# Performance work log

Measured on AMD Instinct MI355X. Metric: run time of the kernel, lower is better.

Reference implementation:

```python
import jax, jax.numpy as jnp
import numpy as np

EMBED, HIDDEN, VOCAB = 512, 512, 30000
B, S, K, NT = 16, 128, 49, 5


def _lin(x, W, b):
    # torch nn.Linear: y = x @ W.T + b, W stored as (out, in)
    return x @ W.T + b


def setup_inputs() -> dict:
    key = jax.random.key(0)
    ks = jax.random.split(key, 32)
    g = lambda i, shape, scale=0.05: (jax.random.normal(ks[i], shape, dtype=jnp.float32) * scale)
    inp = {
        "epoch": 30,
        "h_t": jax.random.normal(ks[0], (B, S, HIDDEN), dtype=jnp.float32),
        "V": jax.random.normal(ks[1], (B, K, HIDDEN), dtype=jnp.float32),
        "T": jax.random.normal(ks[2], (B, NT, EMBED), dtype=jnp.float32),
        "W_ZV": g(3, (49, HIDDEN)), "b_ZV": jnp.zeros((49,), jnp.float32),
        "W_Zh": g(4, (49, HIDDEN)), "b_Zh": jnp.zeros((49,), jnp.float32),
        "W_az": g(5, (1, 49)), "b_az": jnp.zeros((1,), jnp.float32),
        "W_QT": g(6, (5, EMBED)), "b_QT": jnp.zeros((5,), jnp.float32),
        "W_Qh": g(7, (5, HIDDEN)), "b_Qh": jnp.zeros((5,), jnp.float32),
        "W_bq": g(8, (1, 5)), "b_bq": jnp.zeros((1,), jnp.float32),
        "W_sq": g(9, (EMBED, EMBED)), "b_sq": jnp.zeros((EMBED,), jnp.float32),
        "W_sh": g(10, (EMBED, HIDDEN)), "b_sh": jnp.zeros((EMBED,), jnp.float32),
        "W_Ss": g(11, (5, EMBED)), "b_Ss": jnp.zeros((5,), jnp.float32),
        "W_Sr": g(12, (5, EMBED)), "b_Sr": jnp.zeros((5,), jnp.float32),
        "W_sz": g(13, (EMBED, HIDDEN)), "b_sz": jnp.zeros((EMBED,), jnp.float32),
        "W_mlp": g(14, (VOCAB, EMBED)), "b_mlp": jnp.zeros((VOCAB,), jnp.float32),
    }
    return inp


def reference(epoch, h_t, V, T,
              W_ZV, b_ZV, W_Zh, b_Zh, W_az, b_az,
              W_QT, b_QT, W_Qh, b_Qh, W_bq, b_bq,
              W_sq, b_sq, W_sh, b_sh, W_Ss, b_Ss,
              W_Sr, b_Sr, W_sz, b_sz, W_mlp, b_mlp):
    # --- visual attention (dropout = identity, eval mode) ---
    # content_V: [B, S, K, 49]
    content_V = _lin(V, W_ZV, b_ZV)[:, None, :, :] + _lin(h_t, W_Zh, b_Zh)[:, :, None, :]
    visual_t = (jnp.tanh(content_V) @ W_az.T + b_az)[..., 0]          # [B, S, K]
    alpha_t = jax.nn.softmax(visual_t, axis=-1)
    z_t = jnp.einsum('bsk,bkh->bsh', alpha_t, V)                      # [B, S, H]
    r_t = jnp.tanh(_lin(z_t, W_sz, b_sz))                             # [B, S, E]
    # --- topic attention ---
    content_T = _lin(T, W_QT, b_QT)[:, None, :, :] + _lin(h_t, W_Qh, b_Qh)[:, :, None, :]  # [B,S,5,5]
    topic_t = (jnp.tanh(content_T) @ W_bq.T + b_bq)[..., 0]           # [B, S, 5]
    beta_t = jax.nn.softmax(topic_t, axis=-1)
    q_t = jnp.einsum('bst,bte->bse', beta_t, T)                       # [B, S, E]
    s_t = jnp.tanh(_lin(q_t, W_sq, b_sq) + _lin(h_t, W_sh, b_sh))     # [B, S, E]
    # --- sentinel scores: the torch loop reduces to (batch 0, diagonal pos) only ---
    qh0 = _lin(h_t[0], W_Qh, b_Qh)                                    # [S, 5]
    score_s = jnp.tanh(_lin(s_t[0], W_Ss, b_Ss) + qh0) @ W_bq.T + b_bq  # [S, 1]
    score_r = jnp.tanh(_lin(r_t[0], W_Sr, b_Sr) + qh0) @ W_bq.T + b_bq  # [S, 1]
    if epoch <= 20:
        gama_t = 1.0
    else:
        gama_t = jax.nn.sigmoid(score_s - score_r)[None, :, :]        # [1, S, 1]
    c_t = gama_t * s_t + (1.0 - gama_t) * r_t                         # [B, S, E]
    scores = _lin(c_t, W_mlp, b_mlp)                                  # [B, S, vocab]
    return scores
```

## Files before the change

### kernel.cpp

```cpp
#include <hip/hip_runtime.h>
#include <hip/hip_bf16.h>


typedef short bf16x8 __attribute__((ext_vector_type(8)));
typedef float f32x4 __attribute__((ext_vector_type(4)));
typedef short short8 __attribute__((ext_vector_type(8)));

static __device__ __forceinline__ short f2bf(float f) {
    union { float f; unsigned u; } v; v.f = f;
    unsigned r = v.u + 0x7FFFu + ((v.u >> 16) & 1u);
    return (short)(r >> 16);
}

#define GLD_LDS16(gp, lp)                                                          \
    __builtin_amdgcn_global_load_lds(                                              \
        (const __attribute__((address_space(1))) unsigned int*)(gp),               \
        (__attribute__((address_space(3))) unsigned int*)(lp), 16, 0, 0)

__global__ __launch_bounds__(256) void k_front(
    const float* __restrict__ h, const float* __restrict__ V, const float* __restrict__ T,
    const float* __restrict__ W_Zh, const float* __restrict__ b_Zh,
    const float* __restrict__ W_Qh, const float* __restrict__ b_Qh,
    const float* __restrict__ W_ZV, const float* __restrict__ b_ZV,
    const float* __restrict__ W_QT, const float* __restrict__ b_QT,
    float* __restrict__ Zh, float* __restrict__ Qh,
    float* __restrict__ ZV, float* __restrict__ QT,
    const float* __restrict__ wmlp, short* __restrict__ wmlp_b,
    short* __restrict__ h_b,
    const float* __restrict__ wsz, short* __restrict__ wsz_b,
    const float* __restrict__ wsq, short* __restrict__ wsq_b,
    const float* __restrict__ wsh, short* __restrict__ wsh_b)
{
    __shared__ float xs[512];
    const int bid = blockIdx.x;
    const int t = threadIdx.x;

    if (bid < 2048) {
        const float* hp = h + (size_t)bid * 512;
        for (int i = t; i < 512; i += 256) xs[i] = hp[i];
        __syncthreads();
        if (t < 49) {
            const float* w = W_Zh + t * 512;
            float acc = b_Zh[t];
            #pragma unroll 8
            for (int i = 0; i < 512; ++i) acc = fmaf(xs[i], w[i], acc);
            Zh[bid * 64 + t] = acc;
        } else if (t >= 64 && t < 69) {
            const int o = t - 64;
            const float* w = W_Qh + o * 512;
            float acc = b_Qh[o];
            #pragma unroll 8
            for (int i = 0; i < 512; ++i) acc = fmaf(xs[i], w[i], acc);
            Qh[bid * 8 + o] = acc;
        }
        return;
    }
    if (bid < 2912) {
        const int blk = bid - 2048;
        if (blk < 784) {
            const float* xp = V + (size_t)blk * 512;
            for (int i = t; i < 512; i += 256) xs[i] = xp[i];
            __syncthreads();
            if (t < 49) {
                const float* w = W_ZV + t * 512;
                float acc = b_ZV[t];
                #pragma unroll 8
                for (int i = 0; i < 512; ++i) acc = fmaf(xs[i], w[i], acc);
                ZV[blk * 64 + t] = acc;
            }
        } else {
            const int row = blk - 784;
            const float* xp = T + (size_t)row * 512;
            for (int i = t; i < 512; i += 256) xs[i] = xp[i];
            __syncthreads();
            if (t < 5) {
                const float* w = W_QT + t * 512;
                float acc = b_QT[t];
                #pragma unroll 8
                for (int i = 0; i < 512; ++i) acc = fmaf(xs[i], w[i], acc);
                QT[row * 8 + t] = acc;
            }
        }
        return;
    }
    const float* src; short* dst; int i;
    if (bid < 10412)      { src = wmlp; dst = wmlp_b; i = (bid - 2912) * 256 + t; }
    else if (bid < 10924) { src = h;    dst = h_b;    i = (bid - 10412) * 256 + t; }
    else if (bid < 11052) { src = wsz;  dst = wsz_b;  i = (bid - 10924) * 256 + t; }
    else if (bid < 11180) { src = wsq;  dst = wsq_b;  i = (bid - 11052) * 256 + t; }
    else                  { src = wsh;  dst = wsh_b;  i = (bid - 11180) * 256 + t; }
    const float4 a = ((const float4*)src)[i * 2];
    const float4 b = ((const float4*)src)[i * 2 + 1];
    short8 o;
    o[0] = f2bf(a.x); o[1] = f2bf(a.y); o[2] = f2bf(a.z); o[3] = f2bf(a.w);
    o[4] = f2bf(b.x); o[5] = f2bf(b.y); o[6] = f2bf(b.z); o[7] = f2bf(b.w);
    ((short8*)dst)[i] = o;
}

__global__ void k_attn(const float* __restrict__ V, const float* __restrict__ T,
                       const float* __restrict__ ZV, const float* __restrict__ Zh,
                       const float* __restrict__ QT, const float* __restrict__ Qh,
                       const float* __restrict__ W_az, const float* __restrict__ b_az,
                       const float* __restrict__ W_bq, const float* __restrict__ b_bq,
                       short* __restrict__ z_bf, short* __restrict__ q_bf)
{
    const int row = blockIdx.x;
    const int b = row >> 7;
    const int t = threadIdx.x;
    __shared__ float zh[49], waz[49], alpha[49], beta[5];
    if (t < 49) { zh[t] = Zh[row * 64 + t]; waz[t] = W_az[t]; }
    __syncthreads();
    if (t < 49) {
        const float* zv = ZV + (b * 49 + t) * 64;
        float acc = b_az[0];
        for (int j = 0; j < 49; ++j) acc += tanhf(zv[j] + zh[j]) * waz[j];
        alpha[t] = acc;
    } else if (t >= 64 && t < 69) {
        const int tt = t - 64;
        const float* qt = QT + (b * 5 + tt) * 8;
        const float* qh = Qh + row * 8;
        float acc = b_bq[0];
        for (int j = 0; j < 5; ++j) acc += tanhf(qt[j] + qh[j]) * W_bq[j];
        beta[tt] = acc;
    }
    __syncthreads();
    const int wv = t >> 6, l = t & 63;
    if (wv == 0) {
        float a = (l < 49) ? alpha[l] : -1e30f;
        float m = a;
        #pragma unroll
        for (int off = 32; off; off >>= 1) m = fmaxf(m, __shfl_xor(m, off));
        float e = (l < 49) ? expf(a - m) : 0.f;
        float s = e;
        #pragma unroll
        for (int off = 32; off; off >>= 1) s += __shfl_xor(s, off);
        if (l < 49) alpha[l] = e / s;
    } else if (wv == 1) {
        float a = (l < 5) ? beta[l] : -1e30f;
        float m = a;
        #pragma unroll
        for (int off = 32; off; off >>= 1) m = fmaxf(m, __shfl_xor(m, off));
        float e = (l < 5) ? expf(a - m) : 0.f;
        float s = e;
        #pragma unroll
        for (int off = 32; off; off >>= 1) s += __shfl_xor(s, off);
        if (l < 5) beta[l] = e / s;
    }
    __syncthreads();
    const float* Vb = V + (size_t)b * 49 * 512;
    const float* Tb = T + (size_t)b * 5 * 512;
    for (int hd = t; hd < 512; hd += 256) {
        float az = 0.f;
        #pragma unroll
        for (int k = 0; k < 49; ++k) az = fmaf(alpha[k], Vb[k * 512 + hd], az);
        z_bf[(size_t)row * 512 + hd] = f2bf(az);
        float aq = 0.f;
        #pragma unroll
        for (int k = 0; k < 5; ++k) aq = fmaf(beta[k], Tb[k * 512 + hd], aq);
        q_bf[(size_t)row * 512 + hd] = f2bf(aq);
    }
}

__global__ __launch_bounds__(256) void k_rs(
    const short* __restrict__ Zb, const short* __restrict__ Qb, const short* __restrict__ Hb,
    const short* __restrict__ Wsz, const short* __restrict__ Wsq, const short* __restrict__ Wsh,
    const float* __restrict__ b_sz, const float* __restrict__ b_sq, const float* __restrict__ b_sh,
    float* __restrict__ r_t, float* __restrict__ s_t)
{
    constexpr int K = 512, NN = 512;
    __shared__ __align__(16) short sA[64 * 64];
    __shared__ __align__(16) short sW[64 * 64];
    const int tid = threadIdx.x;
    const int l = tid & 63, w = tid >> 6;
    const int m0 = blockIdx.x * 64, n0 = blockIdx.y * 64;
    const int wm = (w & 1) * 32, wn = (w >> 1) * 32;
    const int lm = l & 15, lg = l >> 4;
    const int sr = l >> 3, sc = l & 7;
    f32x4 accr[2][2] = {}, accs[2][2] = {};

#define RS_PASS(AG, WG, ACC)                                                      \
    for (int k0 = 0; k0 < K; k0 += 64) {                                          \
        _Pragma("unroll")                                                         \
        for (int c = 0; c < 2; ++c) {                                             \
            const int R = w * 16 + c * 8;                                         \
            const int row = R + sr;                                               \
            GLD_LDS16((AG) + (size_t)(m0 + row) * K + k0 + ((sc ^ (row & 7)) << 3), sA + R * 64); \
            GLD_LDS16((WG) + (size_t)(n0 + row) * K + k0 + ((sc ^ (row & 7)) << 3), sW + R * 64); \
        }                                                                         \
        __syncthreads();                                                          \
        bf16x8 af[2][2], bv[2][2];                                                \
        _Pragma("unroll")                                                         \
        for (int s = 0; s < 2; ++s)                                               \
            _Pragma("unroll")                                                     \
            for (int i = 0; i < 2; ++i) {                                         \
                const int ra = wm + i * 16 + lm;                                  \
                const int rb = wn + i * 16 + lm;                                  \
                af[s][i] = *(const bf16x8*)(sA + ra * 64 + (((s * 4 + lg) ^ (ra & 7)) << 3)); \
                bv[s][i] = *(const bf16x8*)(sW + rb * 64 + (((s * 4 + lg) ^ (rb & 7)) << 3)); \
            }                                                                     \
        _Pragma("unroll")                                                         \
        for (int s = 0; s < 2; ++s)                                               \
            _Pragma("unroll")                                                     \
            for (int i = 0; i < 2; ++i)                                           \
                _Pragma("unroll")                                                 \
                for (int j = 0; j < 2; ++j)                                       \
                    ACC[i][j] = __builtin_amdgcn_mfma_f32_16x16x32_bf16(af[s][i], bv[s][j], ACC[i][j], 0, 0, 0); \
        __syncthreads();                                                          \
    }

    RS_PASS(Zb, Wsz, accr)
    RS_PASS(Qb, Wsq, accs)
    RS_PASS(Hb, Wsh, accs)
#undef RS_PASS

    #pragma unroll
    for (int j = 0; j < 2; ++j) {
        const int n = n0 + wn + j * 16 + lm;
        const float br = b_sz[n];
        const float bs = b_sq[n] + b_sh[n];
        #pragma unroll
        for (int i = 0; i < 2; ++i) {
            const int m = m0 + wm + i * 16 + lg * 4;
            #pragma unroll
            for (int q = 0; q < 4; ++q) {
                r_t[(size_t)(m + q) * NN + n] = tanhf(accr[i][j][q] + br);
                s_t[(size_t)(m + q) * NN + n] = tanhf(accs[i][j][q] + bs);
            }
        }
    }
}

__global__ __launch_bounds__(256) void k_gemm_mlp(
    const short* __restrict__ A, const short* __restrict__ Wb,
    const float* __restrict__ bias, float* __restrict__ C)
{
    constexpr int N = 30000, K = 512;
    __shared__ __align__(16) short shA[2][128 * 64];
    __shared__ __align__(16) short shW[2][128 * 64];
    const int tid = threadIdx.x;
    const int l = tid & 63, w = tid >> 6;
    const int bid = blockIdx.x;
    const int swz = (bid & 7) * 470 + (bid >> 3);
    const int m0 = (swz & 15) * 128;
    const int n0 = (swz >> 4) * 128;
    const int wm = (w & 1) * 64, wn = (w >> 1) * 64;
    const int lm = l & 15, lg = l >> 4;
    const int sr = tid >> 3, sc = tid & 7;
    const short* Ag = A  + (size_t)m0 * K;
    const short* Wg = Wb + (size_t)n0 * K;
    f32x4 acc[4][4] = {};

#define MLP_STAGE(p, t) {                                                         \
    const int kk = (t) * 64;                                                      \
    _Pragma("unroll")                                                             \
    for (int c = 0; c < 4; ++c) {                                                 \
        const int row = c * 32 + sr;                                              \
        GLD_LDS16(Ag + (size_t)row * K + kk + ((sc ^ (row & 7)) << 3),            \
                  &shA[p][(c * 32 + w * 8) * 64]);                                \
        GLD_LDS16(Wg + (size_t)row * K + kk + ((sc ^ (row & 7)) << 3),            \
                  &shW[p][(c * 32 + w * 8) * 64]);                                \
    } }

#define MLP_STEP(t, vmstr, dostage) {                                             \
    const int p = (t) & 1;                                                        \
    asm volatile(vmstr ::: "memory");                                             \
    __builtin_amdgcn_s_barrier();                                                 \
    bf16x8 af[2][4], bv[2][4];                                                    \
    _Pragma("unroll")                                                             \
    for (int s = 0; s < 2; ++s)                                                   \
      _Pragma("unroll")                                                           \
      for (int i = 0; i < 4; ++i) {                                               \
        const int ra = wm + i * 16 + lm;                                          \
        const int rb = wn + i * 16 + lm;                                          \
        const int ck = s * 4 + lg;                                                \
        af[s][i] = *(const bf16x8*)(&shA[p][ra * 64 + ((ck ^ (ra & 7)) << 3)]);   \
        bv[s][i] = *(const bf16x8*)(&shW[p][rb * 64 + ((ck ^ (rb & 7)) << 3)]);   \
      }                                                                           \
    asm volatile("s_waitcnt lgkmcnt(0)" ::: "memory");                            \
    __builtin_amdgcn_s_barrier();                                                 \
    if (dostage) MLP_STAGE(p, (t) + 2);                                           \
    __builtin_amdgcn_sched_barrier(0);                                            \
    __builtin_amdgcn_s_setprio(1);                                                \
    _Pragma("unroll")                                                             \
    for (int s = 0; s < 2; ++s)                                                   \
      _Pragma("unroll")                                                           \
      for (int i = 0; i < 4; ++i)                                                 \
        _Pragma("unroll")                                                         \
        for (int j = 0; j < 4; ++j)                                               \
            acc[i][j] = __builtin_amdgcn_mfma_f32_16x16x32_bf16(af[s][i], bv[s][j], acc[i][j], 0, 0, 0); \
    __builtin_amdgcn_s_setprio(0);                                                \
  }

    MLP_STAGE(0, 0)
    MLP_STAGE(1, 1)

    MLP_STEP(0, "s_waitcnt vmcnt(8)", 1)
    MLP_STEP(1, "s_waitcnt vmcnt(8)", 1)
    MLP_STEP(2, "s_waitcnt vmcnt(8)", 1)
    MLP_STEP(3, "s_waitcnt vmcnt(8)", 1)
    MLP_STEP(4, "s_waitcnt vmcnt(8)", 1)
    MLP_STEP(5, "s_waitcnt vmcnt(8)", 1)
    MLP_STEP(6, "s_waitcnt vmcnt(8)", 0)
    MLP_STEP(7, "s_waitcnt vmcnt(0)", 0)
#undef MLP_STEP
#undef MLP_STAGE

    #pragma unroll
    for (int j = 0; j < 4; ++j) {
        const int n = n0 + wn + j * 16 + lm;
        if (n >= N) continue;
        const float bj = bias[n];
        #pragma unroll
        for (int i = 0; i < 4; ++i) {
            const int m = m0 + wm + i * 16 + lg * 4;
            #pragma unroll
            for (int q = 0; q < 4; ++q)
                __builtin_nontemporal_store(acc[i][j][q] + bj, &C[(size_t)(m + q) * N + n]);
        }
    }
}

__global__ __launch_bounds__(256) void k_blend_gate(
    const float* __restrict__ s_t, const float* __restrict__ r_t,
    const float* __restrict__ Qh,
    const float* __restrict__ W_Ss, const float* __restrict__ b_Ss,
    const float* __restrict__ W_Sr, const float* __restrict__ b_Sr,
    const float* __restrict__ W_bq, const float* __restrict__ b_bq,
    const int* __restrict__ epoch, short* __restrict__ c_bf)
{
    const int row = blockIdx.x;
    const int s = row & 127;
    const int t = threadIdx.x;
    float g = 1.0f;
    if (epoch[0] > 20) {
        const int l = t & 63;
        const int d = l * 8;
        const float4 s0 = *(const float4*)(s_t + (size_t)s * 512 + d);
        const float4 s1 = *(const float4*)(s_t + (size_t)s * 512 + d + 4);
        const float4 r0 = *(const float4*)(r_t + (size_t)s * 512 + d);
        const float4 r1 = *(const float4*)(r_t + (size_t)s * 512 + d + 4);
        float ss = b_bq[0], sr = b_bq[0];
        #pragma unroll
        for (int k = 0; k < 5; ++k) {
            const float4 w0 = *(const float4*)(W_Ss + k * 512 + d);
            const float4 w1 = *(const float4*)(W_Ss + k * 512 + d + 4);
            const float4 v0 = *(const float4*)(W_Sr + k * 512 + d);
            const float4 v1 = *(const float4*)(W_Sr + k * 512 + d + 4);
            float as = s0.x*w0.x + s0.y*w0.y + s0.z*w0.z + s0.w*w0.w
                     + s1.x*w1.x + s1.y*w1.y + s1.z*w1.z + s1.w*w1.w;
            float ar = r0.x*v0.x + r0.y*v0.y + r0.z*v0.z + r0.w*v0.w
                     + r1.x*v1.x + r1.y*v1.y + r1.z*v1.z + r1.w*v1.w;
            #pragma unroll
            for (int off = 32; off; off >>= 1) {
                as += __shfl_xor(as, off);
                ar += __shfl_xor(ar, off);
            }
            const float qh = Qh[s * 8 + k];
            ss += tanhf(as + b_Ss[k] + qh) * W_bq[k];
            sr += tanhf(ar + b_Sr[k] + qh) * W_bq[k];
        }
        g = 1.f / (1.f + expf(-(ss - sr)));
    }
    const size_t base = (size_t)row * 512;
    for (int i = t; i < 512; i += 256)
        c_bf[base + i] = f2bf(g * s_t[base + i] + (1.f - g) * r_t[base + i]);
}

extern "C" void kernel_launch(void* const* d_in, const int* in_sizes, int n_in,
                              void* d_out, int out_size, void* d_ws, size_t ws_size,
                              hipStream_t stream)
{
    const int*   epoch = (const int*)  d_in[0];
    const float* h_t   = (const float*)d_in[1];
    const float* V     = (const float*)d_in[2];
    const float* T     = (const float*)d_in[3];
    const float* W_ZV  = (const float*)d_in[4];  const float* b_ZV = (const float*)d_in[5];
    const float* W_Zh  = (const float*)d_in[6];  const float* b_Zh = (const float*)d_in[7];
    const float* W_az  = (const float*)d_in[8];  const float* b_az = (const float*)d_in[9];
    const float* W_QT  = (const float*)d_in[10]; const float* b_QT = (const float*)d_in[11];
    const float* W_Qh  = (const float*)d_in[12]; const float* b_Qh = (const float*)d_in[13];
    const float* W_bq  = (const float*)d_in[14]; const float* b_bq = (const float*)d_in[15];
    const float* W_sq  = (const float*)d_in[16]; const float* b_sq = (const float*)d_in[17];
    const float* W_sh  = (const float*)d_in[18]; const float* b_sh = (const float*)d_in[19];
    const float* W_Ss  = (const float*)d_in[20]; const float* b_Ss = (const float*)d_in[21];
    const float* W_Sr  = (const float*)d_in[22]; const float* b_Sr = (const float*)d_in[23];
    const float* W_sz  = (const float*)d_in[24]; const float* b_sz = (const float*)d_in[25];
    const float* W_mlp = (const float*)d_in[26]; const float* b_mlp= (const float*)d_in[27];

    float* out = (float*)d_out;
    float* ws  = (float*)d_ws;
    const size_t M1 = 1024 * 1024;
    float* r_t  = ws;
    float* s_t  = ws + M1;
    float* Zh   = ws + 2 * M1;
    float* ZV   = Zh + 2048 * 64;
    float* Qh   = ZV + 784 * 64;
    float* QT   = Qh + 2048 * 8;
    float* pad  = QT + 80 * 8;
    short* sreg = (short*)(pad + 128);
    short* z_bf   = sreg;
    short* q_bf   = z_bf + M1;
    short* h_bf   = q_bf + M1;
    short* c_bf   = h_bf + M1;
    short* Wsz_bf = c_bf + M1;
    short* Wsq_bf = Wsz_bf + 512 * 512;
    short* Wsh_bf = Wsq_bf + 512 * 512;
    short* W_bf   = Wsh_bf + 512 * 512;

    k_front<<<11308, 256, 0, stream>>>(h_t, V, T,
                                       W_Zh, b_Zh, W_Qh, b_Qh, W_ZV, b_ZV, W_QT, b_QT,
                                       Zh, Qh, ZV, QT,
                                       W_mlp, W_bf, h_bf,
                                       W_sz, Wsz_bf, W_sq, Wsq_bf, W_sh, Wsh_bf);
    k_attn<<<2048, 256, 0, stream>>>(V, T, ZV, Zh, QT, Qh, W_az, b_az, W_bq, b_bq, z_bf, q_bf);
    k_rs<<<dim3(32, 8), 256, 0, stream>>>(z_bf, q_bf, h_bf, Wsz_bf, Wsq_bf, Wsh_bf,
                                          b_sz, b_sq, b_sh, r_t, s_t);
    k_blend_gate<<<2048, 256, 0, stream>>>(s_t, r_t, Qh, W_Ss, b_Ss, W_Sr, b_Sr,
                                           W_bq, b_bq, epoch, c_bf);
    k_gemm_mlp<<<3760, 256, 0, stream>>>(c_bf, W_bf, b_mlp, out);
}
```

Measured before the change: 205.9 us.

## Fuse gate blend into rs GEMM epilogue and stage MLP output through LDS

Adds a small k_gate kernel that recomputes the batch-0 s_t/r_t rows and produces the per-position sentinel gate. The k_rs GEMM then writes the blended bf16 c_t directly, which drops the fp32 r_t/s_t round trip and the separate blend kernel. The MLP GEMM epilogue now stages the accumulators through reused LDS so it can issue coalesced 16-byte nontemporal stores instead of scattered scalar ones. The cost is a serial 128-block gate kernel that recomputes batch-0 work with scalar FMAs, plus an extra LDS pass and barriers in the MLP epilogue.

Result: slower. 250.3 us (+21.5%).

```diff
diff --git a/kernel.cpp b/kernel.cpp
--- a/kernel.cpp
+++ b/kernel.cpp
@@ -10,6 +10,11 @@
     union { float f; unsigned u; } v; v.f = f;
     unsigned r = v.u + 0x7FFFu + ((v.u >> 16) & 1u);
     return (short)(r >> 16);
+}
+static __device__ __forceinline__ float bf2f(short s) {
+    union { unsigned u; float f; } v;
+    v.u = ((unsigned)(unsigned short)s) << 16;
+    return v.f;
 }
 
 #define GLD_LDS16(gp, lp)                                                          \
@@ -161,11 +166,81 @@
     }
 }
 
+__global__ __launch_bounds__(256) void k_gate(
+    const short* __restrict__ Zb, const short* __restrict__ Qb, const short* __restrict__ Hb,
+    const short* __restrict__ Wsz, const short* __restrict__ Wsq, const short* __restrict__ Wsh,
+    const float* __restrict__ b_sz, const float* __restrict__ b_sq, const float* __restrict__ b_sh,
+    const float* __restrict__ Qh,
+    const float* __restrict__ W_Ss, const float* __restrict__ b_Ss,
+    const float* __restrict__ W_Sr, const float* __restrict__ b_Sr,
+    const float* __restrict__ W_bq, const float* __restrict__ b_bq,
+    const int* __restrict__ epoch, float* __restrict__ gama)
+{
+    const int s = blockIdx.x;
+    const int t = threadIdx.x;
+    if (epoch[0] <= 20) { if (t == 0) gama[s] = 1.0f; return; }
+    __shared__ float zs[512], qs[512], hs[512];
+    __shared__ float s0[512], r0[512];
+    for (int i = t; i < 512; i += 256) {
+        zs[i] = bf2f(Zb[(size_t)s * 512 + i]);
+        qs[i] = bf2f(Qb[(size_t)s * 512 + i]);
+        hs[i] = bf2f(Hb[(size_t)s * 512 + i]);
+    }
+    __syncthreads();
+    #pragma unroll
+    for (int half = 0; half < 2; ++half) {
+        const int c = t + half * 256;
+        const short8* wz = (const short8*)(Wsz + (size_t)c * 512);
+        const short8* wq = (const short8*)(Wsq + (size_t)c * 512);
+        const short8* wh = (const short8*)(Wsh + (size_t)c * 512);
+        float ar = b_sz[c];
+        float as = b_sq[c] + b_sh[c];
+        for (int k8 = 0; k8 < 64; ++k8) {
+            const short8 a8 = wz[k8], b8 = wq[k8], c8 = wh[k8];
+            #pragma unroll
+            for (int j = 0; j < 8; ++j) {
+                const int k = k8 * 8 + j;
+                ar = fmaf(zs[k], bf2f(a8[j]), ar);
+                as = fmaf(qs[k], bf2f(b8[j]), as);
+                as = fmaf(hs[k], bf2f(c8[j]), as);
+            }
+        }
+        r0[c] = tanhf(ar);
+        s0[c] = tanhf(as);
+    }
+    __syncthreads();
+    if (t < 64) {
+        const int d = t * 8;
+        float ss = b_bq[0], sr = b_bq[0];
+        #pragma unroll
+        for (int k = 0; k < 5; ++k) {
+            float as = 0.f, ar = 0.f;
+            #pragma unroll
+            for (int j = 0; j < 8; ++j) {
+                const float w = W_Ss[k * 512 + d + j];
+                const float v = W_Sr[k * 512 + d + j];
+                as = fmaf(s0[d + j], w, as);
+                ar = fmaf(r0[d + j], v, ar);
+            }
+            #pragma unroll
+            for (int off = 32; off; off >>= 1) {
+                as += __shfl_xor(as, off);
+                ar += __shfl_xor(ar, off);
+            }
+            const float qh = Qh[s * 8 + k];
+            ss += tanhf(as + b_Ss[k] + qh) * W_bq[k];
+            sr += tanhf(ar + b_Sr[k] + qh) * W_bq[k];
+        }
+        if (t == 0) gama[s] = 1.f / (1.f + expf(-(ss - sr)));
+    }
+}
+
 __global__ __launch_bounds__(256) void k_rs(
     const short* __restrict__ Zb, const short* __restrict__ Qb, const short* __restrict__ Hb,
     const short* __restrict__ Wsz, const short* __restrict__ Wsq, const short* __restrict__ Wsh,
     const float* __restrict__ b_sz, const float* __restrict__ b_sq, const float* __restrict__ b_sh,
-    float* __restrict__ r_t, float* __restrict__ s_t)
+    const float* __restrict__ gama, const int* __restrict__ epoch,
+    short* __restrict__ c_bf)
 {
     constexpr int K = 512, NN = 512;
     __shared__ __align__(16) short sA[64 * 64];
@@ -213,6 +288,7 @@
     RS_PASS(Hb, Wsh, accs)
 #undef RS_PASS
 
+    const int ep = epoch[0];
     #pragma unroll
     for (int j = 0; j < 2; ++j) {
         const int n = n0 + wn + j * 16 + lm;
@@ -223,8 +299,10 @@
             const int m = m0 + wm + i * 16 + lg * 4;
             #pragma unroll
             for (int q = 0; q < 4; ++q) {
-                r_t[(size_t)(m + q) * NN + n] = tanhf(accr[i][j][q] + br);
-                s_t[(size_t)(m + q) * NN + n] = tanhf(accs[i][j][q] + bs);
+                const float rv = tanhf(accr[i][j][q] + br);
+                const float sv = tanhf(accs[i][j][q] + bs);
+                const float g = (ep > 20) ? gama[(m + q) & 127] : 1.0f;
+                c_bf[(size_t)(m + q) * NN + n] = f2bf(g * sv + (1.f - g) * rv);
             }
         }
     }
@@ -235,8 +313,9 @@
     const float* __restrict__ bias, float* __restrict__ C)
 {
     constexpr int N = 30000, K = 512;
-    __shared__ __align__(16) short shA[2][128 * 64];
-    __shared__ __align__(16) short shW[2][128 * 64];
+    __shared__ __align__(16) short lds_s[4][128 * 64];
+#define SHA(p) (lds_s[p])
+#define SHW(p) (lds_s[2 + (p)])
     const int tid = threadIdx.x;
     const int l = tid & 63, w = tid >> 6;
     const int bid = blockIdx.x;
@@ -256,9 +335,9 @@
     for (int c = 0; c < 4; ++c) {                                                 \
         const int row = c * 32 + sr;                                              \
         GLD_LDS16(Ag + (size_t)row * K + kk + ((sc ^ (row & 7)) << 3),            \
-                  &shA[p][(c * 32 + w * 8) * 64]);                                \
+                  &SHA(p)[(c * 32 + w * 8) * 64]);                                \
         GLD_LDS16(Wg + (size_t)row * K + kk + ((sc ^ (row & 7)) << 3),            \
-                  &shW[p][(c * 32 + w * 8) * 64]);                                \
+                  &SHW(p)[(c * 32 + w * 8) * 64]);                                \
     } }
 
 #define MLP_STEP(t, vmstr, dostage) {                                             \
@@ -273,8 +352,8 @@
         const int ra = wm + i * 16 + lm;                                          \
         const int rb = wn + i * 16 + lm;                                          \
         const int ck = s * 4 + lg;                                                \
-        af[s][i] = *(const bf16x8*)(&shA[p][ra * 64 + ((ck ^ (ra & 7)) << 3)]);   \
-        bv[s][i] = *(const bf16x8*)(&shW[p][rb * 64 + ((ck ^ (rb & 7)) << 3)]);   \
+        af[s][i] = *(const bf16x8*)(&SHA(p)[ra * 64 + ((ck ^ (ra & 7)) << 3)]);   \
+        bv[s][i] = *(const bf16x8*)(&SHW(p)[rb * 64 + ((ck ^ (rb & 7)) << 3)]);   \
       }                                                                           \
     asm volatile("s_waitcnt lgkmcnt(0)" ::: "memory");                            \
     __builtin_amdgcn_s_barrier();                                                 \
@@ -305,65 +384,36 @@
 #undef MLP_STEP
 #undef MLP_STAGE
 
+    __syncthreads();
+    float* eld = (float*)&lds_s[0][0];
     #pragma unroll
     for (int j = 0; j < 4; ++j) {
-        const int n = n0 + wn + j * 16 + lm;
-        if (n >= N) continue;
-        const float bj = bias[n];
+        const int nl = wn + j * 16 + lm;
         #pragma unroll
         for (int i = 0; i < 4; ++i) {
-            const int m = m0 + wm + i * 16 + lg * 4;
+            const int ml = wm + i * 16 + lg * 4;
             #pragma unroll
             for (int q = 0; q < 4; ++q)
-                __builtin_nontemporal_store(acc[i][j][q] + bj, &C[(size_t)(m + q) * N + n]);
-        }
-    }
-}
-
-__global__ __launch_bounds__(256) void k_blend_gate(
-    const float* __restrict__ s_t, const float* __restrict__ r_t,
-    const float* __restrict__ Qh,
-    const float* __restrict__ W_Ss, const float* __restrict__ b_Ss,
-    const float* __restrict__ W_Sr, const float* __restrict__ b_Sr,
-    const float* __restrict__ W_bq, const float* __restrict__ b_bq,
-    const int* __restrict__ epoch, short* __restrict__ c_bf)
-{
-    const int row = blockIdx.x;
-    const int s = row & 127;
-    const int t = threadIdx.x;
-    float g = 1.0f;
-    if (epoch[0] > 20) {
-        const int l = t & 63;
-        const int d = l * 8;
-        const float4 s0 = *(const float4*)(s_t + (size_t)s * 512 + d);
-        const float4 s1 = *(const float4*)(s_t + (size_t)s * 512 + d + 4);
-        const float4 r0 = *(const float4*)(r_t + (size_t)s * 512 + d);
-        const float4 r1 = *(const float4*)(r_t + (size_t)s * 512 + d + 4);
-        float ss = b_bq[0], sr = b_bq[0];
-        #pragma unroll
-        for (int k = 0; k < 5; ++k) {
-            const float4 w0 = *(const float4*)(W_Ss + k * 512 + d);
-            const float4 w1 = *(const float4*)(W_Ss + k * 512 + d + 4);
-            const float4 v0 = *(const float4*)(W_Sr + k * 512 + d);
-            const float4 v1 = *(const float4*)(W_Sr + k * 512 + d + 4);
-            float as = s0.x*w0.x + s0.y*w0.y + s0.z*w0.z + s0.w*w0.w
-                     + s1.x*w1.x + s1.y*w1.y + s1.z*w1.z + s1.w*w1.w;
-            float ar = r0.x*v0.x + r0.y*v0.y + r0.z*v0.z + r0.w*v0.w
-                     + r1.x*v1.x + r1.y*v1.y + r1.z*v1.z + r1.w*v1.w;
-            #pragma unroll
-            for (int off = 32; off; off >>= 1) {
-                as += __shfl_xor(as, off);
-                ar += __shfl_xor(ar, off);
-            }
-            const float qh = Qh[s * 8 + k];
-            ss += tanhf(as + b_Ss[k] + qh) * W_bq[k];
-            sr += tanhf(ar + b_Sr[k] + qh) * W_bq[k];
-        }
-        g = 1.f / (1.f + expf(-(ss - sr)));
-    }
-    const size_t base = (size_t)row * 512;
-    for (int i = t; i < 512; i += 256)
-        c_bf[base + i] = f2bf(g * s_t[base + i] + (1.f - g) * r_t[base + i]);
+                eld[(ml + q) * 128 + nl] = acc[i][j][q];
+        }
+    }
+    __syncthreads();
+    #pragma unroll
+    for (int k = 0; k < 16; ++k) {
+        const int flat = k * 256 + tid;
+        const int ml = flat >> 5;
+        const int c4 = (flat & 31) * 4;
+        const int n = n0 + c4;
+        if (n >= N) continue;
+        f32x4 v = *(const f32x4*)(eld + ml * 128 + c4);
+        v[0] += bias[n];
+        v[1] += bias[n + 1];
+        v[2] += bias[n + 2];
+        v[3] += bias[n + 3];
+        __builtin_nontemporal_store(v, (f32x4*)&C[(size_t)(m0 + ml) * N + n]);
+    }
+#undef SHA
+#undef SHW
 }
 
 extern "C" void kernel_launch(void* const* d_in, const int* in_sizes, int n_in,
@@ -390,14 +440,12 @@
     float* out = (float*)d_out;
     float* ws  = (float*)d_ws;
     const size_t M1 = 1024 * 1024;
-    float* r_t  = ws;
-    float* s_t  = ws + M1;
-    float* Zh   = ws + 2 * M1;
+    float* Zh   = ws;
     float* ZV   = Zh + 2048 * 64;
     float* Qh   = ZV + 784 * 64;
     float* QT   = Qh + 2048 * 8;
-    float* pad  = QT + 80 * 8;
-    short* sreg = (short*)(pad + 128);
+    float* gama = QT + 80 * 8;
+    short* sreg = (short*)(gama + 128);
     short* z_bf   = sreg;
     short* q_bf   = z_bf + M1;
     short* h_bf   = q_bf + M1;
@@ -413,9 +461,10 @@
                                        W_mlp, W_bf, h_bf,
                                        W_sz, Wsz_bf, W_sq, Wsq_bf, W_sh, Wsh_bf);
     k_attn<<<2048, 256, 0, stream>>>(V, T, ZV, Zh, QT, Qh, W_az, b_az, W_bq, b_bq, z_bf, q_bf);
+    k_gate<<<128, 256, 0, stream>>>(z_bf, q_bf, h_bf, Wsz_bf, Wsq_bf, Wsh_bf,
+                                    b_sz, b_sq, b_sh, Qh,
+                                    W_Ss, b_Ss, W_Sr, b_Sr, W_bq, b_bq, epoch, gama);
     k_rs<<<dim3(32, 8), 256, 0, stream>>>(z_bf, q_bf, h_bf, Wsz_bf, Wsq_bf, Wsh_bf,
-                                          b_sz, b_sq, b_sh, r_t, s_t);
-    k_blend_gate<<<2048, 256, 0, stream>>>(s_t, r_t, Qh, W_Ss, b_Ss, W_Sr, b_Sr,
-                                           W_bq, b_bq, epoch, c_bf);
+                                          b_sz, b_sq, b_sh, gama, epoch, c_bf);
     k_gemm_mlp<<<3760, 256, 0, stream>>>(c_bf, W_bf, b_mlp, out);
 }
```

## Replace double-buffered MLP GEMM pipeline with single-buffer loop and higher occupancy

Applied to the files above, without the earlier changes.

Removes the hand-scheduled two-stage LDS prefetch pipeline in the vocab projection GEMM and replaces it with a plain loop: load a K-tile, sync, compute, sync. LDS use per block is halved and launch bounds request 4 blocks per CU, so more blocks can co-reside and hide latency through occupancy instead of explicit prefetch. In exchange, load and compute within a block are no longer overlapped, and the s_setprio hints and fine-grained waitcnt control are dropped.

Result: faster. 197.9 us (-3.9%).

```diff
diff --git a/kernel.cpp b/kernel.cpp
--- a/kernel.cpp
+++ b/kernel.cpp
@@ -230,13 +230,13 @@
     }
 }
 
-__global__ __launch_bounds__(256) void k_gemm_mlp(
+__global__ __launch_bounds__(256, 4) void k_gemm_mlp(
     const short* __restrict__ A, const short* __restrict__ Wb,
     const float* __restrict__ bias, float* __restrict__ C)
 {
     constexpr int N = 30000, K = 512;
-    __shared__ __align__(16) short shA[2][128 * 64];
-    __shared__ __align__(16) short shW[2][128 * 64];
+    __shared__ __align__(16) short shA[128 * 64];
+    __shared__ __align__(16) short shW[128 * 64];
     const int tid = threadIdx.x;
     const int l = tid & 63, w = tid >> 6;
     const int bid = blockIdx.x;
@@ -250,60 +250,38 @@
     const short* Wg = Wb + (size_t)n0 * K;
     f32x4 acc[4][4] = {};
 
-#define MLP_STAGE(p, t) {                                                         \
-    const int kk = (t) * 64;                                                      \
-    _Pragma("unroll")                                                             \
-    for (int c = 0; c < 4; ++c) {                                                 \
-        const int row = c * 32 + sr;                                              \
-        GLD_LDS16(Ag + (size_t)row * K + kk + ((sc ^ (row & 7)) << 3),            \
-                  &shA[p][(c * 32 + w * 8) * 64]);                                \
-        GLD_LDS16(Wg + (size_t)row * K + kk + ((sc ^ (row & 7)) << 3),            \
-                  &shW[p][(c * 32 + w * 8) * 64]);                                \
-    } }
-
-#define MLP_STEP(t, vmstr, dostage) {                                             \
-    const int p = (t) & 1;                                                        \
-    asm volatile(vmstr ::: "memory");                                             \
-    __builtin_amdgcn_s_barrier();                                                 \
-    bf16x8 af[2][4], bv[2][4];                                                    \
-    _Pragma("unroll")                                                             \
-    for (int s = 0; s < 2; ++s)                                                   \
-      _Pragma("unroll")                                                           \
-      for (int i = 0; i < 4; ++i) {                                               \
-        const int ra = wm + i * 16 + lm;                                          \
-        const int rb = wn + i * 16 + lm;                                          \
-        const int ck = s * 4 + lg;                                                \
-        af[s][i] = *(const bf16x8*)(&shA[p][ra * 64 + ((ck ^ (ra & 7)) << 3)]);   \
-        bv[s][i] = *(const bf16x8*)(&shW[p][rb * 64 + ((ck ^ (rb & 7)) << 3)]);   \
-      }                                                                           \
-    asm volatile("s_waitcnt lgkmcnt(0)" ::: "memory");                            \
-    __builtin_amdgcn_s_barrier();                                                 \
-    if (dostage) MLP_STAGE(p, (t) + 2);                                           \
-    __builtin_amdgcn_sched_barrier(0);                                            \
-    __builtin_amdgcn_s_setprio(1);                                                \
-    _Pragma("unroll")                                                             \
-    for (int s = 0; s < 2; ++s)                                                   \
-      _Pragma("unroll")                                                           \
-      for (int i = 0; i < 4; ++i)                                                 \
-        _Pragma("unroll")                                                         \
-        for (int j = 0; j < 4; ++j)                                               \
-            acc[i][j] = __builtin_amdgcn_mfma_f32_16x16x32_bf16(af[s][i], bv[s][j], acc[i][j], 0, 0, 0); \
-    __builtin_amdgcn_s_setprio(0);                                                \
-  }
-
-    MLP_STAGE(0, 0)
-    MLP_STAGE(1, 1)
-
-    MLP_STEP(0, "s_waitcnt vmcnt(8)", 1)
-    MLP_STEP(1, "s_waitcnt vmcnt(8)", 1)
-    MLP_STEP(2, "s_waitcnt vmcnt(8)", 1)
-    MLP_STEP(3, "s_waitcnt vmcnt(8)", 1)
-    MLP_STEP(4, "s_waitcnt vmcnt(8)", 1)
-    MLP_STEP(5, "s_waitcnt vmcnt(8)", 1)
-    MLP_STEP(6, "s_waitcnt vmcnt(8)", 0)
-    MLP_STEP(7, "s_waitcnt vmcnt(0)", 0)
-#undef MLP_STEP
-#undef MLP_STAGE
+    for (int t = 0; t < 8; ++t) {
+        const int kk = t * 64;
+        #pragma unroll
+        for (int c = 0; c < 4; ++c) {
+            const int row = c * 32 + sr;
+            GLD_LDS16(Ag + (size_t)row * K + kk + ((sc ^ (row & 7)) << 3),
+                      &shA[(c * 32 + w * 8) * 64]);
+            GLD_LDS16(Wg + (size_t)row * K + kk + ((sc ^ (row & 7)) << 3),
+                      &shW[(c * 32 + w * 8) * 64]);
+        }
+        __syncthreads();
+        bf16x8 af[2][4], bv[2][4];
+        #pragma unroll
+        for (int s = 0; s < 2; ++s)
+            #pragma unroll
+            for (int i = 0; i < 4; ++i) {
+                const int ra = wm + i * 16 + lm;
+                const int rb = wn + i * 16 + lm;
+                const int ck = s * 4 + lg;
+                af[s][i] = *(const bf16x8*)(&shA[ra * 64 + ((ck ^ (ra & 7)) << 3)]);
+                bv[s][i] = *(const bf16x8*)(&shW[rb * 64 + ((ck ^ (rb & 7)) << 3)]);
+            }
+        #pragma unroll
+        for (int s = 0; s < 2; ++s)
+            #pragma unroll
+            for (int i = 0; i < 4; ++i)
+                #pragma unroll
+                for (int j = 0; j < 4; ++j)
+                    acc[i][j] = __builtin_amdgcn_mfma_f32_16x16x32_bf16(
+                        af[s][i], bv[s][j], acc[i][j], 0, 0, 0);
+        __syncthreads();
+    }
 
     #pragma unroll
     for (int j = 0; j < 4; ++j) {
```
